# Kernel optimization log

Measured on AMD Instinct MI355X. Metric: run time of the kernel, lower is better.

Reference implementation:

```python
import jax, jax.numpy as jnp
import numpy as np
from jax import lax

B, T, N, HID = 4, 144, 256, 64
CH, NC = 9, 4  # chunk_size_short, num_chunks_short


def setup_inputs():
    key = jax.random.key(0)
    ks = jax.random.split(key, 30)
    r = lambda i, sh, s=0.05: jax.random.normal(ks[i], sh, jnp.float32) * s
    adj = (jax.random.uniform(ks[1], (N, N)) < 0.1).astype(jnp.float32)
    adj = adj.at[jnp.arange(N), jnp.arange(N)].set(1.0)  # self-loops
    return {
        "seg": jax.random.normal(ks[0], (B, T, N, N), jnp.float32),
        "adj": adj,
        "dist": jax.random.uniform(ks[2], (N, N), jnp.float32),
        "W_gat": r(3, (N, HID)),
        "a_src": r(4, (HID,)),
        "a_dst": r(5, (HID,)),
        "lstm_Wih": r(6, (4 * HID, HID)),
        "lstm_Whh": r(7, (4 * HID, HID)),
        "lstm_bih": r(8, (4 * HID,)),
        "lstm_bhh": r(9, (4 * HID,)),
        "attnL_W": r(10, (HID, HID)),
        "attnL_b": r(11, (HID,)),
        "attnL_v": r(12, (HID,)),
        "gru_Wih": r(13, (NC, 3 * HID, HID)),
        "gru_Whh": r(14, (NC, 3 * HID, HID)),
        "gru_bih": r(15, (NC, 3 * HID)),
        "gru_bhh": r(16, (NC, 3 * HID)),
        "attnS_W": r(17, (NC, HID, HID)),
        "attnS_b": r(18, (NC, HID)),
        "attnS_v": r(19, (NC, HID)),
        "lin1_W": r(20, (2 * HID, HID + HID * NC)),
        "lin1_b": r(21, (2 * HID,)),
        "lin2_W": r(22, (N * N, 2 * HID)),
        "lin2_b": r(23, (N * N,)),
        "conv_k": r(24, (1, 1, 3, 3)),
        "conv_b": r(25, (1,)),
    }


def gat_features(seg, adj, dist, W_gat, a_src, a_dst):
    # Batches the per-timestep GAT over the time axis (B,T folded together).
    Wh = jnp.einsum('btnf,fh->btnh', seg, W_gat)                     # (B,T,N,H)
    e = jax.nn.leaky_relu((Wh @ a_src)[..., :, None] + (Wh @ a_dst)[..., None, :], 0.2)
    e = e - dist                                                     # distance penalty on logits
    logits = jnp.where(adj > 0, e, -1e9)                             # mask non-edges
    attn = jax.nn.softmax(logits, axis=-1)                           # (B,T,N,N)
    Hn = jax.nn.elu(jnp.einsum('btij,btjh->btih', attn, Wh))         # (B,T,N,H)
    return Hn.mean(axis=2)                                           # (B,T,H) mean-pool over nodes


def lstm(x, Wih, Whh, bih, bhh):
    h0 = jnp.zeros((x.shape[0], Whh.shape[1]), x.dtype)
    def step(carry, xt):
        h, c = carry
        g = xt @ Wih.T + bih + h @ Whh.T + bhh
        i, f, gg, o = jnp.split(g, 4, axis=-1)  # torch gate order i,f,g,o
        c = jax.nn.sigmoid(f) * c + jax.nn.sigmoid(i) * jnp.tanh(gg)
        h = jax.nn.sigmoid(o) * jnp.tanh(c)
        return (h, c), h
    _, ys = lax.scan(step, (h0, h0), jnp.swapaxes(x, 0, 1))
    return jnp.swapaxes(ys, 0, 1)


def gru(x, Wih, Whh, bih, bhh):
    h0 = jnp.zeros((x.shape[0], Whh.shape[1]), x.dtype)
    def step(h, xt):
        gx = xt @ Wih.T + bih
        gh = h @ Whh.T + bhh
        xr, xz, xn = jnp.split(gx, 3, axis=-1)  # torch gate order r,z,n
        hr, hz, hn = jnp.split(gh, 3, axis=-1)
        rr = jax.nn.sigmoid(xr + hr)
        zz = jax.nn.sigmoid(xz + hz)
        nn_ = jnp.tanh(xn + rr * hn)
        h = (1.0 - zz) * nn_ + zz * h
        return h, h
    _, ys = lax.scan(step, h0, jnp.swapaxes(x, 0, 1))
    return jnp.swapaxes(ys, 0, 1)


def tattn(h, W, b, v):
    s = jnp.tanh(h @ W + b) @ v          # (B,T) additive attention scores
    a = jax.nn.softmax(s, axis=1)
    return jnp.einsum('bt,bth->bh', a, h)


def reference(seg, adj, dist, W_gat, a_src, a_dst, lstm_Wih, lstm_Whh, lstm_bih, lstm_bhh,
              attnL_W, attnL_b, attnL_v, gru_Wih, gru_Whh, gru_bih, gru_bhh,
              attnS_W, attnS_b, attnS_v, lin1_W, lin1_b, lin2_W, lin2_b, conv_k, conv_b):
    Bsz = seg.shape[0]
    feats = gat_features(seg, adj, dist, W_gat, a_src, a_dst)        # (B,T,H)
    ctxL = tattn(lstm(feats, lstm_Wih, lstm_Whh, lstm_bih, lstm_bhh), attnL_W, attnL_b, attnL_v)
    # Short-term GCN features are the same GAT outputs on the last W_short steps.
    short = feats[:, -CH * NC:, :].reshape(Bsz, NC, CH, HID)
    gru_out = jax.vmap(gru, in_axes=(1, 0, 0, 0, 0), out_axes=1)(short, gru_Wih, gru_Whh, gru_bih, gru_bhh)
    ctxS = jax.vmap(tattn, in_axes=(1, 0, 0, 0), out_axes=1)(gru_out, attnS_W, attnS_b, attnS_v)  # (B,NC,H)
    fused = jnp.concatenate([ctxL, ctxS.reshape(Bsz, NC * HID)], axis=1)  # (B, 5H)
    h1 = jax.nn.relu(fused @ lin1_W.T + lin1_b)
    out = (h1 @ lin2_W.T + lin2_b).reshape(Bsz, 1, N, N)
    out = lax.conv_general_dilated(out, conv_k, (1, 1), 'SAME',
                                   dimension_numbers=('NCHW', 'OIHW', 'NCHW'))
    out = out + conv_b[None, :, None, None]
    return jax.nn.softplus(out[:, 0])
```

## Files before the change

### kernel.cpp

```cpp
#include <hip/hip_runtime.h>
#include <hip/hip_bf16.h>
#include <cstddef>


typedef __attribute__((ext_vector_type(8))) short bf16x8;
typedef __attribute__((ext_vector_type(4))) float f32x4;

__device__ __forceinline__ float sigf(float x) { return 1.0f / (1.0f + __expf(-x)); }
__device__ __forceinline__ float tanh_(float x) {
    x = fminf(fmaxf(x, -15.f), 15.f);
    float e = __expf(2.f * x);
    return (e - 1.f) / (e + 1.f);
}
__device__ __forceinline__ unsigned short f2b(float f) {
    unsigned u = __float_as_uint(f);
    u += 0x7FFFu + ((u >> 16) & 1u);
    return (unsigned short)(u >> 16);
}
__device__ __forceinline__ unsigned pk2(float lo, float hi) {
    __hip_bfloat162 h = __float22bfloat162_rn(float2{lo, hi});
    return *reinterpret_cast<unsigned*>(&h);
}
__device__ __forceinline__ float b2f(short s) {
    return __uint_as_float(((unsigned)(unsigned short)s) << 16);
}

__global__ void k_prep(const float* __restrict__ adj, const float* __restrict__ dist,
                       const float* __restrict__ W_gat,
                       unsigned short* __restrict__ Mb, unsigned short* __restrict__ Wt) {
    int blk = blockIdx.x, tid = threadIdx.x;
    if (blk < 256) {
        int i = blk * 256 + tid;
        Mb[i] = f2b((adj[i] > 0.f) ? -dist[i] : -1e9f);
    } else {
        for (int it = 0; it < 64; ++it) {
            int e = it * 256 + tid;
            int k = e >> 6, c = e & 63;
            Wt[c * 256 + k] = f2b(W_gat[e]);
        }
    }
}

__global__ __launch_bounds__(256, 3) void k_gat(
    const float* __restrict__ seg, const unsigned short* __restrict__ Wt,
    const float* __restrict__ a_src, const float* __restrict__ a_dst,
    const unsigned short* __restrict__ Mb, float* __restrict__ feats,
    const float* __restrict__ lWih, const float* __restrict__ lbih,
    const float* __restrict__ lbhh, float* __restrict__ gx) {
    __shared__ __align__(16) short AB_s[256 * 64];
    __shared__ __align__(16) float svec[256];
    __shared__ __align__(16) float dvec[256];
    __shared__ __align__(16) float red[256];
    __shared__ __align__(16) float feats_l[64];

    const int tid  = threadIdx.x;
    const int lane = tid & 63;
    const int wv   = tid >> 6;
    const int wrow = wv * 64;
    const int bt   = blockIdx.x;
    const float* __restrict__ segp = seg + (size_t)bt * 65536;

    f32x4 acc[4][4];
    #pragma unroll
    for (int a = 0; a < 4; ++a)
        #pragma unroll
        for (int b = 0; b < 4; ++b) acc[a][b] = (f32x4)(0.f);

    for (int kc = 0; kc < 4; ++kc) {
        #pragma unroll
        for (int it = 0; it < 8; ++it) {
            int unit = it * 256 + tid;
            int row = unit >> 3, u = unit & 7;
            const float* g = segp + row * 256 + kc * 64 + u * 8;
            f32x4 v0 = *(const f32x4*)g;
            f32x4 v1 = *(const f32x4*)(g + 4);
            uint4 pk;
            pk.x = pk2(v0[0], v0[1]); pk.y = pk2(v0[2], v0[3]);
            pk.z = pk2(v1[0], v1[1]); pk.w = pk2(v1[2], v1[3]);
            *(uint4*)&AB_s[(row * 8 + (u ^ (row & 7))) * 8] = pk;
        }
        bf16x8 bfr[2][4];
        #pragma unroll
        for (int kt2 = 0; kt2 < 2; ++kt2) {
            int ku = kt2 * 4 + (lane >> 4);
            #pragma unroll
            for (int nt = 0; nt < 4; ++nt) {
                int col = nt * 16 + (lane & 15);
                bfr[kt2][nt] = *(const bf16x8*)(Wt + col * 256 + kc * 64 + ku * 8);
            }
        }
        __syncthreads();
        #pragma unroll
        for (int kt2 = 0; kt2 < 2; ++kt2) {
            int ku = kt2 * 4 + (lane >> 4);
            #pragma unroll
            for (int mt = 0; mt < 4; ++mt) {
                int row = wrow + mt * 16 + (lane & 15);
                bf16x8 afr = *(const bf16x8*)&AB_s[(row * 8 + (ku ^ (row & 7))) * 8];
                #pragma unroll
                for (int nt = 0; nt < 4; ++nt)
                    acc[mt][nt] = __builtin_amdgcn_mfma_f32_16x16x32_bf16(afr, bfr[kt2][nt], acc[mt][nt], 0, 0, 0);
            }
        }
        __syncthreads();
    }

    float asv[4], adv[4];
    #pragma unroll
    for (int nt = 0; nt < 4; ++nt) {
        asv[nt] = a_src[nt * 16 + (lane & 15)];
        adv[nt] = a_dst[nt * 16 + (lane & 15)];
    }
    #pragma unroll
    for (int mt = 0; mt < 4; ++mt) {
        #pragma unroll
        for (int r = 0; r < 4; ++r) {
            float ps = acc[mt][0][r] * asv[0] + acc[mt][1][r] * asv[1]
                     + acc[mt][2][r] * asv[2] + acc[mt][3][r] * asv[3];
            float pd = acc[mt][0][r] * adv[0] + acc[mt][1][r] * adv[1]
                     + acc[mt][2][r] * adv[2] + acc[mt][3][r] * adv[3];
            #pragma unroll
            for (int m = 1; m < 16; m <<= 1) {
                ps += __shfl_xor(ps, m);
                pd += __shfl_xor(pd, m);
            }
            if ((lane & 15) == 0) {
                int row = wrow + mt * 16 + (lane >> 4) * 4 + r;
                svec[row] = ps;
                dvec[row] = pd;
            }
        }
        #pragma unroll
        for (int nt = 0; nt < 4; ++nt) {
            int col  = nt * 16 + (lane & 15);
            int row0 = wrow + mt * 16 + (lane >> 4) * 4;
            uint2 pk4;
            pk4.x = pk2(acc[mt][nt][0], acc[mt][nt][1]);
            pk4.y = pk2(acc[mt][nt][2], acc[mt][nt][3]);
            int addr16 = col * 32 + ((row0 >> 3) ^ (col & 7));
            *(uint2*)&AB_s[addr16 * 8 + (row0 & 7)] = pk4;
        }
    }
    __syncthreads();

    {
        float a = svec[tid], b = dvec[tid];
        #pragma unroll
        for (int m = 1; m < 64; m <<= 1) {
            a = fmaxf(a, __shfl_xor(a, m));
            b = fmaxf(b, __shfl_xor(b, m));
        }
        if (lane == 0) { red[wv] = a; red[4 + wv] = b; }
    }
    __syncthreads();
    float mB;
    {
        float ms = fmaxf(fmaxf(red[0], red[1]), fmaxf(red[2], red[3]));
        float md = fmaxf(fmaxf(red[4], red[5]), fmaxf(red[6], red[7]));
        float x = ms + md;
        mB = fmaxf(x, 0.2f * x);
    }

    f32x4 acc2[4][4];
    #pragma unroll
    for (int a = 0; a < 4; ++a)
        #pragma unroll
        for (int b = 0; b < 4; ++b) acc2[a][b] = (f32x4)(0.f);
    float psum[4] = {0.f, 0.f, 0.f, 0.f};
    float sv4[4];
    #pragma unroll
    for (int mt = 0; mt < 4; ++mt) sv4[mt] = svec[wrow + mt * 16 + (lane & 15)];
    const int jbase = (lane >> 4) * 8;
    #pragma unroll 1
    for (int kt = 0; kt < 8; ++kt) {
        int j0 = kt * 32 + jbase;
        int ku = kt * 4 + (lane >> 4);
        bf16x8 bfr2[4];
        #pragma unroll
        for (int nt = 0; nt < 4; ++nt) {
            int col = nt * 16 + (lane & 15);
            bfr2[nt] = *(const bf16x8*)&AB_s[(col * 32 + (ku ^ (col & 7))) * 8];
        }
        f32x4 dv0 = *(const f32x4*)&dvec[j0];
        f32x4 dv1 = *(const f32x4*)&dvec[j0 + 4];
        #pragma unroll
        for (int mt = 0; mt < 4; ++mt) {
            int row = wrow + mt * 16 + (lane & 15);
            bf16x8 mrow = *(const bf16x8*)(Mb + row * 256 + j0);
            float p[8];
            #pragma unroll
            for (int e = 0; e < 4; ++e) {
                float u = sv4[mt] + dv0[e];
                u = fmaxf(u, 0.2f * u);
                p[e] = __expf(u + b2f(mrow[e]) - mB);
                float w = sv4[mt] + dv1[e];
                w = fmaxf(w, 0.2f * w);
                p[4 + e] = __expf(w + b2f(mrow[4 + e]) - mB);
            }
            psum[mt] += ((p[0] + p[1]) + (p[2] + p[3])) + ((p[4] + p[5]) + (p[6] + p[7]));
            uint4 upf;
            upf.x = pk2(p[0], p[1]); upf.y = pk2(p[2], p[3]);
            upf.z = pk2(p[4], p[5]); upf.w = pk2(p[6], p[7]);
            bf16x8 pf = *reinterpret_cast<bf16x8*>(&upf);
            #pragma unroll
            for (int nt = 0; nt < 4; ++nt)
                acc2[mt][nt] = __builtin_amdgcn_mfma_f32_16x16x32_bf16(pf, bfr2[nt], acc2[mt][nt], 0, 0, 0);
        }
    }
    #pragma unroll
    for (int mt = 0; mt < 4; ++mt) {
        psum[mt] += __shfl_xor(psum[mt], 16);
        psum[mt] += __shfl_xor(psum[mt], 32);
    }

    float part[4] = {0.f, 0.f, 0.f, 0.f};
    #pragma unroll
    for (int mt = 0; mt < 4; ++mt) {
        #pragma unroll
        for (int r = 0; r < 4; ++r) {
            float rs  = __shfl(psum[mt], ((lane >> 4) << 2) + r);
            float inv = 1.0f / rs;
            #pragma unroll
            for (int nt = 0; nt < 4; ++nt) {
                float x = acc2[mt][nt][r] * inv;
                x = (x > 0.f) ? x : expm1f(x);
                part[nt] += x;
            }
        }
    }
    #pragma unroll
    for (int nt = 0; nt < 4; ++nt) {
        part[nt] += __shfl_xor(part[nt], 16);
        part[nt] += __shfl_xor(part[nt], 32);
    }
    if ((lane >> 4) == 0) {
        #pragma unroll
        for (int nt = 0; nt < 4; ++nt) red[wv * 64 + nt * 16 + lane] = part[nt];
    }
    __syncthreads();
    if (tid < 64) {
        float f = (red[tid] + red[64 + tid] + red[128 + tid] + red[192 + tid]) * (1.0f / 256.0f);
        feats[bt * 64 + tid] = f;
        feats_l[tid] = f;
    }
    __syncthreads();

    {
        float a = lbih[tid] + lbhh[tid];
        const float* wp = lWih + tid * 64;
        #pragma unroll
        for (int k4 = 0; k4 < 16; ++k4) {
            f32x4 w = *(const f32x4*)(wp + k4 * 4);
            f32x4 x = *(const f32x4*)&feats_l[k4 * 4];
            a += w[0] * x[0] + w[1] * x[1] + w[2] * x[2] + w[3] * x[3];
        }
        gx[bt * 256 + tid] = a;
    }
}

__global__ __launch_bounds__(256) void k_rnn(
    const float* __restrict__ gx, const float* __restrict__ lWhh, float* __restrict__ lout,
    const float* __restrict__ feats, const float* __restrict__ gWih,
    const float* __restrict__ gWhh, const float* __restrict__ gbih,
    const float* __restrict__ gbhh, float* __restrict__ gout) {
    int tid = threadIdx.x;
    if (blockIdx.x < 4) {
        int b = blockIdx.x;
        int lane = tid & 63, wv = tid >> 6;
        __shared__ __align__(16) float hv[4][64];
        __shared__ __align__(16) float gl[2][256];
        float wr[64];
        #pragma unroll
        for (int q = 0; q < 16; ++q)
            *(f32x4*)&wr[q * 4] = *(const f32x4*)&lWhh[tid * 64 + q * 4];
        float c_s = 0.f;
        hv[wv][lane] = 0.f;
        for (int t = 0; t < 144; ++t) {
            float a = gx[(b * 144 + t) * 256 + tid];
            #pragma unroll
            for (int q = 0; q < 16; ++q) {
                f32x4 h4 = *(const f32x4*)&hv[wv][q * 4];
                a += wr[q * 4 + 0] * h4[0] + wr[q * 4 + 1] * h4[1]
                   + wr[q * 4 + 2] * h4[2] + wr[q * 4 + 3] * h4[3];
            }
            gl[t & 1][tid] = a;
            __syncthreads();
            float ig = gl[t & 1][lane],       fg = gl[t & 1][64 + lane],
                  gg = gl[t & 1][128 + lane], og = gl[t & 1][192 + lane];
            c_s = sigf(fg) * c_s + sigf(ig) * tanh_(gg);
            float h = sigf(og) * tanh_(c_s);
            hv[wv][lane] = h;
            if (wv == 0) lout[(b * 144 + t) * 64 + lane] = h;
        }
    } else {
        int bi_ = blockIdx.x - 4;
        int b = bi_ >> 2, c2 = bi_ & 3;
        __shared__ float hvg[64], xvg[64], gxl[192], ghl[192];
        float wi[64], wh[64], bi = 0.f, bh = 0.f, h_s = 0.f;
        if (tid < 192) {
            #pragma unroll
            for (int q = 0; q < 16; ++q) {
                *(f32x4*)&wi[q * 4] = *(const f32x4*)&gWih[(size_t)(c2 * 192 + tid) * 64 + q * 4];
                *(f32x4*)&wh[q * 4] = *(const f32x4*)&gWhh[(size_t)(c2 * 192 + tid) * 64 + q * 4];
            }
            bi = gbih[c2 * 192 + tid];
            bh = gbhh[c2 * 192 + tid];
        }
        if (tid < 64) hvg[tid] = 0.f;
        __syncthreads();
        for (int s = 0; s < 9; ++s) {
            int t = 108 + c2 * 9 + s;
            if (tid < 64) xvg[tid] = feats[(b * 144 + t) * 64 + tid];
            __syncthreads();
            if (tid < 192) {
                float ax = bi, ah = bh;
                #pragma unroll
                for (int k = 0; k < 64; ++k) { ax += wi[k] * xvg[k]; ah += wh[k] * hvg[k]; }
                gxl[tid] = ax; ghl[tid] = ah;
            }
            __syncthreads();
            if (tid < 64) {
                float xr = gxl[tid], xz = gxl[64 + tid], xn = gxl[128 + tid];
                float hr = ghl[tid], hz = ghl[64 + tid], hn = ghl[128 + tid];
                float rr = sigf(xr + hr), zz = sigf(xz + hz);
                float nn = tanh_(xn + rr * hn);
                h_s = (1.f - zz) * nn + zz * h_s;
                hvg[tid] = h_s;
                gout[((b * 4 + c2) * 9 + s) * 64 + tid] = h_s;
            }
            __syncthreads();
        }
    }
}

__global__ __launch_bounds__(256) void k_ctx(
    const float* __restrict__ lout, const float* __restrict__ aLW,
    const float* __restrict__ aLb, const float* __restrict__ aLv,
    const float* __restrict__ gout, const float* __restrict__ aSW,
    const float* __restrict__ aSb, const float* __restrict__ aSv,
    float* __restrict__ ctxL, float* __restrict__ ctxS) {
    int tid = threadIdx.x;
    if (blockIdx.x < 4) {
        int b = blockIdx.x;
        int wv = tid >> 6, lane = tid & 63;
        __shared__ __align__(16) float Hl[144 * 64];
        __shared__ float sc[144];
        __shared__ float al[144];
        for (int i = tid; i < 9216; i += 256) Hl[i] = lout[b * 9216 + i];
        float wcol[64];
        #pragma unroll
        for (int k = 0; k < 64; ++k) wcol[k] = aLW[k * 64 + lane];
        float bb = aLb[lane], vv = aLv[lane];
        __syncthreads();
        for (int g = 0; g < 36; ++g) {
            int t = g * 4 + wv;
            float acc = bb;
            #pragma unroll
            for (int q = 0; q < 16; ++q) {
                f32x4 h4 = *(const f32x4*)&Hl[t * 64 + q * 4];
                acc += wcol[q * 4 + 0] * h4[0] + wcol[q * 4 + 1] * h4[1]
                     + wcol[q * 4 + 2] * h4[2] + wcol[q * 4 + 3] * h4[3];
            }
            float p = tanh_(acc) * vv;
            #pragma unroll
            for (int m = 1; m < 64; m <<= 1) p += __shfl_xor(p, m);
            if (lane == 0) sc[t] = p;
        }
        __syncthreads();
        float mx = -3e38f;
        for (int t2 = 0; t2 < 144; ++t2) mx = fmaxf(mx, sc[t2]);
        float ss = 0.f;
        for (int t2 = 0; t2 < 144; ++t2) ss += __expf(sc[t2] - mx);
        float inv = 1.f / ss;
        if (tid < 144) al[tid] = __expf(sc[tid] - mx) * inv;
        __syncthreads();
        if (tid < 64) {
            float acc = 0.f;
            for (int t2 = 0; t2 < 144; ++t2) acc += al[t2] * Hl[t2 * 64 + tid];
            ctxL[b * 64 + tid] = acc;
        }
    } else {
        int bi_ = blockIdx.x - 4;
        int b = bi_ >> 2, c2 = bi_ & 3;
        __shared__ float xv2[64];
        if (tid < 64) {
            int lane = tid;
            const float* Wc = aSW + c2 * 4096;
            float wcol[64];
            #pragma unroll
            for (int k = 0; k < 64; ++k) wcol[k] = Wc[k * 64 + lane];
            float bb = aSb[c2 * 64 + lane], vv = aSv[c2 * 64 + lane];
            float sv[9], hl[9];
            #pragma unroll 1
            for (int s = 0; s < 9; ++s) {
                float h = gout[((size_t)((b * 4 + c2) * 9 + s)) * 64 + lane];
                hl[s] = h;
                xv2[lane] = h;
                float acc = bb;
                #pragma unroll
                for (int k = 0; k < 64; ++k) acc += wcol[k] * xv2[k];
                float p = tanh_(acc) * vv;
                #pragma unroll
                for (int m = 1; m < 64; m <<= 1) p += __shfl_xor(p, m);
                sv[s] = p;
            }
            float mx = -3e38f;
            #pragma unroll
            for (int s = 0; s < 9; ++s) mx = fmaxf(mx, sv[s]);
            float ss = 0.f;
            #pragma unroll
            for (int s = 0; s < 9; ++s) { sv[s] = __expf(sv[s] - mx); ss += sv[s]; }
            float inv = 1.f / ss;
            float acc = 0.f;
            #pragma unroll
            for (int s = 0; s < 9; ++s) acc += sv[s] * inv * hl[s];
            ctxS[(b * 4 + c2) * 64 + lane] = acc;
        }
    }
}

__global__ __launch_bounds__(512) void k_lin1(
    const float* __restrict__ ctxL, const float* __restrict__ ctxS,
    const float* __restrict__ W, const float* __restrict__ bb,
    float* __restrict__ h1) {
    int tid = threadIdx.x;
    __shared__ __align__(16) float fu[4 * 320];
    for (int c = tid; c < 1280; c += 512) {
        int b2 = c / 320, k = c % 320;
        fu[c] = (k < 64) ? ctxL[b2 * 64 + k] : ctxS[b2 * 256 + (k - 64)];
    }
    __syncthreads();
    int b = tid >> 7, r = tid & 127;
    float acc = bb[r];
    #pragma unroll 4
    for (int k4 = 0; k4 < 80; ++k4) {
        f32x4 w = *(const f32x4*)&W[r * 320 + k4 * 4];
        f32x4 x = *(const f32x4*)&fu[b * 320 + k4 * 4];
        acc += w[0] * x[0] + w[1] * x[1] + w[2] * x[2] + w[3] * x[3];
    }
    h1[b * 128 + r] = fmaxf(acc, 0.f);
}

__global__ __launch_bounds__(256) void k_lin2(
    const float* __restrict__ h1, const float* __restrict__ W,
    const float* __restrict__ bb, float* __restrict__ h2) {
    int tid = threadIdx.x, blk = blockIdx.x;
    __shared__ __align__(16) float Wc[128 * 132];
    __shared__ __align__(16) float h1l[512];
    __shared__ __align__(16) float red2[512];
    for (int c = tid; c < 512; c += 256) h1l[c] = h1[c];
    #pragma unroll
    for (int it = 0; it < 16; ++it) {
        int flat = it * 1024 + tid * 4;
        int row = flat >> 7, col = flat & 127;
        f32x4 v = *(const f32x4*)&W[(size_t)(blk * 128 + row) * 128 + col];
        *(f32x4*)&Wc[row * 132 + col] = v;
    }
    __syncthreads();
    int r2 = tid >> 1, half = tid & 1;
    float a0 = 0.f, a1 = 0.f, a2 = 0.f, a3 = 0.f;
    #pragma unroll
    for (int i = 0; i < 16; ++i) {
        f32x4 w = *(const f32x4*)&Wc[r2 * 132 + half * 64 + i * 4];
        f32x4 x0 = *(const f32x4*)&h1l[half * 64 + i * 4];
        f32x4 x1 = *(const f32x4*)&h1l[128 + half * 64 + i * 4];
        f32x4 x2 = *(const f32x4*)&h1l[256 + half * 64 + i * 4];
        f32x4 x3 = *(const f32x4*)&h1l[384 + half * 64 + i * 4];
        a0 += w[0] * x0[0] + w[1] * x0[1] + w[2] * x0[2] + w[3] * x0[3];
        a1 += w[0] * x1[0] + w[1] * x1[1] + w[2] * x1[2] + w[3] * x1[3];
        a2 += w[0] * x2[0] + w[1] * x2[1] + w[2] * x2[2] + w[3] * x2[3];
        a3 += w[0] * x3[0] + w[1] * x3[1] + w[2] * x3[2] + w[3] * x3[3];
    }
    if (half == 1) {
        f32x4 v; v[0] = a0; v[1] = a1; v[2] = a2; v[3] = a3;
        *(f32x4*)&red2[r2 * 4] = v;
    }
    __syncthreads();
    if (half == 0) {
        f32x4 v = *(const f32x4*)&red2[r2 * 4];
        int r = blk * 128 + r2;
        float bv = bb[r];
        h2[r]              = a0 + v[0] + bv;
        h2[65536 + r]      = a1 + v[1] + bv;
        h2[2 * 65536 + r]  = a2 + v[2] + bv;
        h2[3 * 65536 + r]  = a3 + v[3] + bv;
    }
}

__global__ __launch_bounds__(256) void k_conv(
    const float* __restrict__ h2, const float* __restrict__ ck,
    const float* __restrict__ cb, float* __restrict__ out) {
    int x = threadIdx.x;
    int b = blockIdx.x >> 8, y = blockIdx.x & 255;
    float kk[9];
    #pragma unroll
    for (int i = 0; i < 9; ++i) kk[i] = ck[i];
    const float* base = h2 + b * 65536;
    float acc = cb[0];
    #pragma unroll
    for (int dy = -1; dy <= 1; ++dy) {
        int yy = y + dy;
        if (yy < 0 || yy > 255) continue;
        #pragma unroll
        for (int dx = -1; dx <= 1; ++dx) {
            int xx = x + dx;
            if (xx < 0 || xx > 255) continue;
            acc += base[yy * 256 + xx] * kk[(dy + 1) * 3 + (dx + 1)];
        }
    }
    float r = (acc > 20.f) ? acc : log1pf(__expf(acc));
    out[b * 65536 + y * 256 + x] = r;
}

extern "C" void kernel_launch(void* const* d_in, const int* in_sizes, int n_in,
                              void* d_out, int out_size, void* d_ws, size_t ws_size,
                              hipStream_t stream) {
    const float* seg   = (const float*)d_in[0];
    const float* adj   = (const float*)d_in[1];
    const float* dist  = (const float*)d_in[2];
    const float* W_gat = (const float*)d_in[3];
    const float* a_src = (const float*)d_in[4];
    const float* a_dst = (const float*)d_in[5];
    const float* lWih  = (const float*)d_in[6];
    const float* lWhh  = (const float*)d_in[7];
    const float* lbih  = (const float*)d_in[8];
    const float* lbhh  = (const float*)d_in[9];
    const float* aLW   = (const float*)d_in[10];
    const float* aLb   = (const float*)d_in[11];
    const float* aLv   = (const float*)d_in[12];
    const float* gWih  = (const float*)d_in[13];
    const float* gWhh  = (const float*)d_in[14];
    const float* gbih  = (const float*)d_in[15];
    const float* gbhh  = (const float*)d_in[16];
    const float* aSW   = (const float*)d_in[17];
    const float* aSb   = (const float*)d_in[18];
    const float* aSv   = (const float*)d_in[19];
    const float* l1W   = (const float*)d_in[20];
    const float* l1b   = (const float*)d_in[21];
    const float* l2W   = (const float*)d_in[22];
    const float* l2b   = (const float*)d_in[23];
    const float* ck    = (const float*)d_in[24];
    const float* cb    = (const float*)d_in[25];
    float* out = (float*)d_out;

    float* ws    = (float*)d_ws;
    unsigned short* Mb = (unsigned short*)ws;
    float* feats = ws + 32768;
    float* gx    = feats + 36864;
    float* lout  = gx + 147456;
    float* ctxL  = lout + 36864;
    float* gout  = ctxL + 256;
    float* ctxS  = gout + 9216;
    float* h1    = ctxS + 1024;
    float* h2    = h1 + 512;
    unsigned short* Wt = (unsigned short*)(h2 + 262144);

    k_prep<<<257, 256, 0, stream>>>(adj, dist, W_gat, Mb, Wt);
    k_gat<<<576, 256, 0, stream>>>(seg, Wt, a_src, a_dst, Mb, feats, lWih, lbih, lbhh, gx);
    k_rnn<<<20, 256, 0, stream>>>(gx, lWhh, lout, feats, gWih, gWhh, gbih, gbhh, gout);
    k_ctx<<<20, 256, 0, stream>>>(lout, aLW, aLb, aLv, gout, aSW, aSb, aSv, ctxL, ctxS);
    k_lin1<<<1, 512, 0, stream>>>(ctxL, ctxS, l1W, l1b, h1);
    k_lin2<<<512, 256, 0, stream>>>(h1, l2W, l2b, h2);
    k_conv<<<1024, 256, 0, stream>>>(h2, ck, cb, out);
}
```

Before: 236.2 us.

## Split GAT kernel into row-block projection and attention kernels, tweak RNN and lin2

Splits the fused per-timestep GAT kernel into k_gatA (projection of 64 rows per block, writing Wh transposed plus source/destination scores and partial maxima to global memory) and k_gatB (attention aggregation of 64 rows per block). A new k_feats kernel reduces the four partial pools and applies the LSTM input projection. The aim is to raise the block count from 576 to 2304 and cut per-block LDS and register use so more blocks fit per CU. The cost is global round-trips for Wh and the score vectors plus two extra launches. It also prefetches gx and splits accumulators in the LSTM/GRU loops, and makes lin2 read weights directly from global with shuffle reductions instead of staging through LDS.

Result: slower. 272.1 us (+15.2%).

```diff
diff --git a/kernel.cpp b/kernel.cpp
--- a/kernel.cpp
+++ b/kernel.cpp
@@ -41,34 +41,29 @@
     }
 }
 
-__global__ __launch_bounds__(256, 3) void k_gat(
+__global__ __launch_bounds__(256, 6) void k_gatA(
     const float* __restrict__ seg, const unsigned short* __restrict__ Wt,
     const float* __restrict__ a_src, const float* __restrict__ a_dst,
-    const unsigned short* __restrict__ Mb, float* __restrict__ feats,
-    const float* __restrict__ lWih, const float* __restrict__ lbih,
-    const float* __restrict__ lbhh, float* __restrict__ gx) {
-    __shared__ __align__(16) short AB_s[256 * 64];
-    __shared__ __align__(16) float svec[256];
-    __shared__ __align__(16) float dvec[256];
-    __shared__ __align__(16) float red[256];
-    __shared__ __align__(16) float feats_l[64];
+    unsigned short* __restrict__ WhT, float* __restrict__ svec, float* __restrict__ dvec,
+    float* __restrict__ smaxp, float* __restrict__ dmaxp) {
+    __shared__ __align__(16) short A_s[64 * 64];
+    __shared__ float red[8];
 
     const int tid  = threadIdx.x;
     const int lane = tid & 63;
     const int wv   = tid >> 6;
-    const int wrow = wv * 64;
-    const int bt   = blockIdx.x;
-    const float* __restrict__ segp = seg + (size_t)bt * 65536;
-
-    f32x4 acc[4][4];
-    #pragma unroll
-    for (int a = 0; a < 4; ++a)
-        #pragma unroll
-        for (int b = 0; b < 4; ++b) acc[a][b] = (f32x4)(0.f);
+    const int blk  = blockIdx.x;
+    const int bt   = blk >> 2;
+    const int sub  = blk & 3;
+    const float* __restrict__ segp = seg + (size_t)bt * 65536 + sub * 64 * 256;
+
+    f32x4 acc[4];
+    #pragma unroll
+    for (int n = 0; n < 4; ++n) acc[n] = (f32x4)(0.f);
 
     for (int kc = 0; kc < 4; ++kc) {
         #pragma unroll
-        for (int it = 0; it < 8; ++it) {
+        for (int it = 0; it < 2; ++it) {
             int unit = it * 256 + tid;
             int row = unit >> 3, u = unit & 7;
             const float* g = segp + row * 256 + kc * 64 + u * 8;
@@ -77,7 +72,7 @@
             uint4 pk;
             pk.x = pk2(v0[0], v0[1]); pk.y = pk2(v0[2], v0[3]);
             pk.z = pk2(v1[0], v1[1]); pk.w = pk2(v1[2], v1[3]);
-            *(uint4*)&AB_s[(row * 8 + (u ^ (row & 7))) * 8] = pk;
+            *(uint4*)&A_s[(row * 8 + (u ^ (row & 7))) * 8] = pk;
         }
         bf16x8 bfr[2][4];
         #pragma unroll
@@ -90,17 +85,14 @@
             }
         }
         __syncthreads();
+        int arow = wv * 16 + (lane & 15);
         #pragma unroll
         for (int kt2 = 0; kt2 < 2; ++kt2) {
             int ku = kt2 * 4 + (lane >> 4);
-            #pragma unroll
-            for (int mt = 0; mt < 4; ++mt) {
-                int row = wrow + mt * 16 + (lane & 15);
-                bf16x8 afr = *(const bf16x8*)&AB_s[(row * 8 + (ku ^ (row & 7))) * 8];
-                #pragma unroll
-                for (int nt = 0; nt < 4; ++nt)
-                    acc[mt][nt] = __builtin_amdgcn_mfma_f32_16x16x32_bf16(afr, bfr[kt2][nt], acc[mt][nt], 0, 0, 0);
-            }
+            bf16x8 afr = *(const bf16x8*)&A_s[(arow * 8 + (ku ^ (arow & 7))) * 8];
+            #pragma unroll
+            for (int nt = 0; nt < 4; ++nt)
+                acc[nt] = __builtin_amdgcn_mfma_f32_16x16x32_bf16(afr, bfr[kt2][nt], acc[nt], 0, 0, 0);
         }
         __syncthreads();
     }
@@ -111,121 +103,123 @@
         asv[nt] = a_src[nt * 16 + (lane & 15)];
         adv[nt] = a_dst[nt * 16 + (lane & 15)];
     }
-    #pragma unroll
-    for (int mt = 0; mt < 4; ++mt) {
-        #pragma unroll
-        for (int r = 0; r < 4; ++r) {
-            float ps = acc[mt][0][r] * asv[0] + acc[mt][1][r] * asv[1]
-                     + acc[mt][2][r] * asv[2] + acc[mt][3][r] * asv[3];
-            float pd = acc[mt][0][r] * adv[0] + acc[mt][1][r] * adv[1]
-                     + acc[mt][2][r] * adv[2] + acc[mt][3][r] * adv[3];
-            #pragma unroll
-            for (int m = 1; m < 16; m <<= 1) {
-                ps += __shfl_xor(ps, m);
-                pd += __shfl_xor(pd, m);
-            }
-            if ((lane & 15) == 0) {
-                int row = wrow + mt * 16 + (lane >> 4) * 4 + r;
-                svec[row] = ps;
-                dvec[row] = pd;
-            }
-        }
+    float mxs = -3e38f, mxd = -3e38f;
+    int rowbase = sub * 64 + wv * 16;
+    #pragma unroll
+    for (int r = 0; r < 4; ++r) {
+        float ps = acc[0][r] * asv[0] + acc[1][r] * asv[1] + acc[2][r] * asv[2] + acc[3][r] * asv[3];
+        float pd = acc[0][r] * adv[0] + acc[1][r] * adv[1] + acc[2][r] * adv[2] + acc[3][r] * adv[3];
+        #pragma unroll
+        for (int m = 1; m < 16; m <<= 1) { ps += __shfl_xor(ps, m); pd += __shfl_xor(pd, m); }
+        if ((lane & 15) == 0) {
+            int row = rowbase + (lane >> 4) * 4 + r;
+            svec[bt * 256 + row] = ps;
+            dvec[bt * 256 + row] = pd;
+        }
+        mxs = fmaxf(mxs, ps); mxd = fmaxf(mxd, pd);
+    }
+    {
+        unsigned short* Wp = WhT + (size_t)bt * 16384;
+        int row0 = rowbase + (lane >> 4) * 4;
         #pragma unroll
         for (int nt = 0; nt < 4; ++nt) {
-            int col  = nt * 16 + (lane & 15);
-            int row0 = wrow + mt * 16 + (lane >> 4) * 4;
+            int col = nt * 16 + (lane & 15);
             uint2 pk4;
-            pk4.x = pk2(acc[mt][nt][0], acc[mt][nt][1]);
-            pk4.y = pk2(acc[mt][nt][2], acc[mt][nt][3]);
-            int addr16 = col * 32 + ((row0 >> 3) ^ (col & 7));
-            *(uint2*)&AB_s[addr16 * 8 + (row0 & 7)] = pk4;
-        }
-    }
+            pk4.x = pk2(acc[nt][0], acc[nt][1]);
+            pk4.y = pk2(acc[nt][2], acc[nt][3]);
+            *(uint2*)(Wp + col * 256 + row0) = pk4;
+        }
+    }
+    mxs = fmaxf(mxs, __shfl_xor(mxs, 16)); mxs = fmaxf(mxs, __shfl_xor(mxs, 32));
+    mxd = fmaxf(mxd, __shfl_xor(mxd, 16)); mxd = fmaxf(mxd, __shfl_xor(mxd, 32));
+    if (lane == 0) { red[wv] = mxs; red[4 + wv] = mxd; }
     __syncthreads();
-
-    {
-        float a = svec[tid], b = dvec[tid];
-        #pragma unroll
-        for (int m = 1; m < 64; m <<= 1) {
-            a = fmaxf(a, __shfl_xor(a, m));
-            b = fmaxf(b, __shfl_xor(b, m));
-        }
-        if (lane == 0) { red[wv] = a; red[4 + wv] = b; }
-    }
-    __syncthreads();
+    if (tid == 0) {
+        smaxp[blk] = fmaxf(fmaxf(red[0], red[1]), fmaxf(red[2], red[3]));
+        dmaxp[blk] = fmaxf(fmaxf(red[4], red[5]), fmaxf(red[6], red[7]));
+    }
+}
+
+__global__ __launch_bounds__(256, 4) void k_gatB(
+    const unsigned short* __restrict__ WhT, const float* __restrict__ svec,
+    const float* __restrict__ dvec, const float* __restrict__ smaxp,
+    const float* __restrict__ dmaxp, const unsigned short* __restrict__ Mb,
+    float* __restrict__ fpart) {
+    __shared__ __align__(16) float dv_l[256];
+    __shared__ float red[256];
+
+    const int tid  = threadIdx.x;
+    const int lane = tid & 63;
+    const int wv   = tid >> 6;
+    const int blk  = blockIdx.x;
+    const int bt   = blk >> 2;
+    const int sub  = blk & 3;
+    const unsigned short* __restrict__ Wp = WhT + (size_t)bt * 16384;
+
+    dv_l[tid] = dvec[bt * 256 + tid];
     float mB;
     {
-        float ms = fmaxf(fmaxf(red[0], red[1]), fmaxf(red[2], red[3]));
-        float md = fmaxf(fmaxf(red[4], red[5]), fmaxf(red[6], red[7]));
+        float ms = fmaxf(fmaxf(smaxp[bt * 4], smaxp[bt * 4 + 1]),
+                         fmaxf(smaxp[bt * 4 + 2], smaxp[bt * 4 + 3]));
+        float md = fmaxf(fmaxf(dmaxp[bt * 4], dmaxp[bt * 4 + 1]),
+                         fmaxf(dmaxp[bt * 4 + 2], dmaxp[bt * 4 + 3]));
         float x = ms + md;
         mB = fmaxf(x, 0.2f * x);
     }
-
-    f32x4 acc2[4][4];
-    #pragma unroll
-    for (int a = 0; a < 4; ++a)
-        #pragma unroll
-        for (int b = 0; b < 4; ++b) acc2[a][b] = (f32x4)(0.f);
-    float psum[4] = {0.f, 0.f, 0.f, 0.f};
-    float sv4[4];
-    #pragma unroll
-    for (int mt = 0; mt < 4; ++mt) sv4[mt] = svec[wrow + mt * 16 + (lane & 15)];
+    const int prow = sub * 64 + wv * 16 + (lane & 15);
+    const float sv = svec[bt * 256 + prow];
+    __syncthreads();
+
+    f32x4 acc2[4];
+    #pragma unroll
+    for (int n = 0; n < 4; ++n) acc2[n] = (f32x4)(0.f);
+    float psum = 0.f;
     const int jbase = (lane >> 4) * 8;
+
     #pragma unroll 1
     for (int kt = 0; kt < 8; ++kt) {
         int j0 = kt * 32 + jbase;
-        int ku = kt * 4 + (lane >> 4);
-        bf16x8 bfr2[4];
+        bf16x8 bfr[4];
         #pragma unroll
         for (int nt = 0; nt < 4; ++nt) {
             int col = nt * 16 + (lane & 15);
-            bfr2[nt] = *(const bf16x8*)&AB_s[(col * 32 + (ku ^ (col & 7))) * 8];
-        }
-        f32x4 dv0 = *(const f32x4*)&dvec[j0];
-        f32x4 dv1 = *(const f32x4*)&dvec[j0 + 4];
-        #pragma unroll
-        for (int mt = 0; mt < 4; ++mt) {
-            int row = wrow + mt * 16 + (lane & 15);
-            bf16x8 mrow = *(const bf16x8*)(Mb + row * 256 + j0);
-            float p[8];
-            #pragma unroll
-            for (int e = 0; e < 4; ++e) {
-                float u = sv4[mt] + dv0[e];
-                u = fmaxf(u, 0.2f * u);
-                p[e] = __expf(u + b2f(mrow[e]) - mB);
-                float w = sv4[mt] + dv1[e];
-                w = fmaxf(w, 0.2f * w);
-                p[4 + e] = __expf(w + b2f(mrow[4 + e]) - mB);
-            }
-            psum[mt] += ((p[0] + p[1]) + (p[2] + p[3])) + ((p[4] + p[5]) + (p[6] + p[7]));
-            uint4 upf;
-            upf.x = pk2(p[0], p[1]); upf.y = pk2(p[2], p[3]);
-            upf.z = pk2(p[4], p[5]); upf.w = pk2(p[6], p[7]);
-            bf16x8 pf = *reinterpret_cast<bf16x8*>(&upf);
-            #pragma unroll
-            for (int nt = 0; nt < 4; ++nt)
-                acc2[mt][nt] = __builtin_amdgcn_mfma_f32_16x16x32_bf16(pf, bfr2[nt], acc2[mt][nt], 0, 0, 0);
-        }
-    }
-    #pragma unroll
-    for (int mt = 0; mt < 4; ++mt) {
-        psum[mt] += __shfl_xor(psum[mt], 16);
-        psum[mt] += __shfl_xor(psum[mt], 32);
-    }
+            bfr[nt] = *(const bf16x8*)(Wp + col * 256 + j0);
+        }
+        bf16x8 mrow = *(const bf16x8*)(Mb + prow * 256 + j0);
+        f32x4 d0 = *(const f32x4*)&dv_l[j0];
+        f32x4 d1 = *(const f32x4*)&dv_l[j0 + 4];
+        float p[8];
+        #pragma unroll
+        for (int e = 0; e < 4; ++e) {
+            float u = sv + d0[e];
+            u = fmaxf(u, 0.2f * u);
+            p[e] = __expf(u + b2f(mrow[e]) - mB);
+            float w = sv + d1[e];
+            w = fmaxf(w, 0.2f * w);
+            p[4 + e] = __expf(w + b2f(mrow[4 + e]) - mB);
+        }
+        psum += ((p[0] + p[1]) + (p[2] + p[3])) + ((p[4] + p[5]) + (p[6] + p[7]));
+        uint4 upf;
+        upf.x = pk2(p[0], p[1]); upf.y = pk2(p[2], p[3]);
+        upf.z = pk2(p[4], p[5]); upf.w = pk2(p[6], p[7]);
+        bf16x8 pf = *reinterpret_cast<bf16x8*>(&upf);
+        #pragma unroll
+        for (int nt = 0; nt < 4; ++nt)
+            acc2[nt] = __builtin_amdgcn_mfma_f32_16x16x32_bf16(pf, bfr[nt], acc2[nt], 0, 0, 0);
+    }
+    psum += __shfl_xor(psum, 16);
+    psum += __shfl_xor(psum, 32);
 
     float part[4] = {0.f, 0.f, 0.f, 0.f};
     #pragma unroll
-    for (int mt = 0; mt < 4; ++mt) {
-        #pragma unroll
-        for (int r = 0; r < 4; ++r) {
-            float rs  = __shfl(psum[mt], ((lane >> 4) << 2) + r);
-            float inv = 1.0f / rs;
-            #pragma unroll
-            for (int nt = 0; nt < 4; ++nt) {
-                float x = acc2[mt][nt][r] * inv;
-                x = (x > 0.f) ? x : expm1f(x);
-                part[nt] += x;
-            }
+    for (int r = 0; r < 4; ++r) {
+        float rs  = __shfl(psum, ((lane >> 4) << 2) + r);
+        float inv = 1.0f / rs;
+        #pragma unroll
+        for (int nt = 0; nt < 4; ++nt) {
+            float x = acc2[nt][r] * inv;
+            x = (x > 0.f) ? x : expm1f(x);
+            part[nt] += x;
         }
     }
     #pragma unroll
@@ -238,24 +232,32 @@
         for (int nt = 0; nt < 4; ++nt) red[wv * 64 + nt * 16 + lane] = part[nt];
     }
     __syncthreads();
+    if (tid < 64)
+        fpart[blk * 64 + tid] = red[tid] + red[64 + tid] + red[128 + tid] + red[192 + tid];
+}
+
+__global__ __launch_bounds__(256) void k_feats(
+    const float* __restrict__ fpart, const float* __restrict__ lWih,
+    const float* __restrict__ lbih, const float* __restrict__ lbhh,
+    float* __restrict__ feats, float* __restrict__ gx) {
+    __shared__ __align__(16) float fl[64];
+    int bt = blockIdx.x, tid = threadIdx.x;
     if (tid < 64) {
-        float f = (red[tid] + red[64 + tid] + red[128 + tid] + red[192 + tid]) * (1.0f / 256.0f);
+        float f = (fpart[(bt * 4 + 0) * 64 + tid] + fpart[(bt * 4 + 1) * 64 + tid]
+                 + fpart[(bt * 4 + 2) * 64 + tid] + fpart[(bt * 4 + 3) * 64 + tid]) * (1.0f / 256.0f);
         feats[bt * 64 + tid] = f;
-        feats_l[tid] = f;
+        fl[tid] = f;
     }
     __syncthreads();
-
-    {
-        float a = lbih[tid] + lbhh[tid];
-        const float* wp = lWih + tid * 64;
-        #pragma unroll
-        for (int k4 = 0; k4 < 16; ++k4) {
-            f32x4 w = *(const f32x4*)(wp + k4 * 4);
-            f32x4 x = *(const f32x4*)&feats_l[k4 * 4];
-            a += w[0] * x[0] + w[1] * x[1] + w[2] * x[2] + w[3] * x[3];
-        }
-        gx[bt * 256 + tid] = a;
-    }
+    float a = lbih[tid] + lbhh[tid];
+    const float* wp = lWih + tid * 64;
+    #pragma unroll
+    for (int k4 = 0; k4 < 16; ++k4) {
+        f32x4 w = *(const f32x4*)(wp + k4 * 4);
+        f32x4 x = *(const f32x4*)&fl[k4 * 4];
+        a += w[0] * x[0] + w[1] * x[1] + w[2] * x[2] + w[3] * x[3];
+    }
+    gx[bt * 256 + tid] = a;
 }
 
 __global__ __launch_bounds__(256) void k_rnn(
@@ -275,14 +277,22 @@
             *(f32x4*)&wr[q * 4] = *(const f32x4*)&lWhh[tid * 64 + q * 4];
         float c_s = 0.f;
         hv[wv][lane] = 0.f;
+        float gx_cur = gx[(size_t)b * 144 * 256 + tid];
         for (int t = 0; t < 144; ++t) {
-            float a = gx[(b * 144 + t) * 256 + tid];
-            #pragma unroll
-            for (int q = 0; q < 16; ++q) {
-                f32x4 h4 = *(const f32x4*)&hv[wv][q * 4];
-                a += wr[q * 4 + 0] * h4[0] + wr[q * 4 + 1] * h4[1]
-                   + wr[q * 4 + 2] * h4[2] + wr[q * 4 + 3] * h4[3];
-            }
+            float gx_next = (t < 143) ? gx[((size_t)b * 144 + t + 1) * 256 + tid] : 0.f;
+            float s0 = 0.f, s1 = 0.f, s2 = 0.f, s3 = 0.f;
+            #pragma unroll
+            for (int q = 0; q < 4; ++q) {
+                f32x4 h0 = *(const f32x4*)&hv[wv][q * 16];
+                f32x4 h1 = *(const f32x4*)&hv[wv][q * 16 + 4];
+                f32x4 h2 = *(const f32x4*)&hv[wv][q * 16 + 8];
+                f32x4 h3 = *(const f32x4*)&hv[wv][q * 16 + 12];
+                s0 += wr[q*16+ 0]*h0[0] + wr[q*16+ 1]*h0[1] + wr[q*16+ 2]*h0[2] + wr[q*16+ 3]*h0[3];
+                s1 += wr[q*16+ 4]*h1[0] + wr[q*16+ 5]*h1[1] + wr[q*16+ 6]*h1[2] + wr[q*16+ 7]*h1[3];
+                s2 += wr[q*16+ 8]*h2[0] + wr[q*16+ 9]*h2[1] + wr[q*16+10]*h2[2] + wr[q*16+11]*h2[3];
+                s3 += wr[q*16+12]*h3[0] + wr[q*16+13]*h3[1] + wr[q*16+14]*h3[2] + wr[q*16+15]*h3[3];
+            }
+            float a = gx_cur + ((s0 + s1) + (s2 + s3));
             gl[t & 1][tid] = a;
             __syncthreads();
             float ig = gl[t & 1][lane],       fg = gl[t & 1][64 + lane],
@@ -291,6 +301,7 @@
             float h = sigf(og) * tanh_(c_s);
             hv[wv][lane] = h;
             if (wv == 0) lout[(b * 144 + t) * 64 + lane] = h;
+            gx_cur = gx_next;
         }
     } else {
         int bi_ = blockIdx.x - 4;
@@ -314,9 +325,13 @@
             __syncthreads();
             if (tid < 192) {
                 float ax = bi, ah = bh;
+                float a0 = 0.f, a1 = 0.f, b0 = 0.f, b1 = 0.f;
                 #pragma unroll
-                for (int k = 0; k < 64; ++k) { ax += wi[k] * xvg[k]; ah += wh[k] * hvg[k]; }
-                gxl[tid] = ax; ghl[tid] = ah;
+                for (int k = 0; k < 64; k += 2) {
+                    a0 += wi[k] * xvg[k];     a1 += wi[k + 1] * xvg[k + 1];
+                    b0 += wh[k] * hvg[k];     b1 += wh[k + 1] * hvg[k + 1];
+                }
+                gxl[tid] = ax + a0 + a1; ghl[tid] = ah + b0 + b1;
             }
             __syncthreads();
             if (tid < 64) {
@@ -444,46 +459,36 @@
 __global__ __launch_bounds__(256) void k_lin2(
     const float* __restrict__ h1, const float* __restrict__ W,
     const float* __restrict__ bb, float* __restrict__ h2) {
+    __shared__ __align__(16) float h1l[512];
     int tid = threadIdx.x, blk = blockIdx.x;
-    __shared__ __align__(16) float Wc[128 * 132];
-    __shared__ __align__(16) float h1l[512];
-    __shared__ __align__(16) float red2[512];
     for (int c = tid; c < 512; c += 256) h1l[c] = h1[c];
-    #pragma unroll
-    for (int it = 0; it < 16; ++it) {
-        int flat = it * 1024 + tid * 4;
-        int row = flat >> 7, col = flat & 127;
-        f32x4 v = *(const f32x4*)&W[(size_t)(blk * 128 + row) * 128 + col];
-        *(f32x4*)&Wc[row * 132 + col] = v;
-    }
     __syncthreads();
-    int r2 = tid >> 1, half = tid & 1;
+    int r = blk * 64 + (tid >> 2);
+    int q = tid & 3;
+    const float* wp = W + (size_t)r * 128 + q * 32;
     float a0 = 0.f, a1 = 0.f, a2 = 0.f, a3 = 0.f;
     #pragma unroll
-    for (int i = 0; i < 16; ++i) {
-        f32x4 w = *(const f32x4*)&Wc[r2 * 132 + half * 64 + i * 4];
-        f32x4 x0 = *(const f32x4*)&h1l[half * 64 + i * 4];
-        f32x4 x1 = *(const f32x4*)&h1l[128 + half * 64 + i * 4];
-        f32x4 x2 = *(const f32x4*)&h1l[256 + half * 64 + i * 4];
-        f32x4 x3 = *(const f32x4*)&h1l[384 + half * 64 + i * 4];
+    for (int i = 0; i < 8; ++i) {
+        f32x4 w  = *(const f32x4*)(wp + i * 4);
+        f32x4 x0 = *(const f32x4*)&h1l[q * 32 + i * 4];
+        f32x4 x1 = *(const f32x4*)&h1l[128 + q * 32 + i * 4];
+        f32x4 x2 = *(const f32x4*)&h1l[256 + q * 32 + i * 4];
+        f32x4 x3 = *(const f32x4*)&h1l[384 + q * 32 + i * 4];
         a0 += w[0] * x0[0] + w[1] * x0[1] + w[2] * x0[2] + w[3] * x0[3];
         a1 += w[0] * x1[0] + w[1] * x1[1] + w[2] * x1[2] + w[3] * x1[3];
         a2 += w[0] * x2[0] + w[1] * x2[1] + w[2] * x2[2] + w[3] * x2[3];
         a3 += w[0] * x3[0] + w[1] * x3[1] + w[2] * x3[2] + w[3] * x3[3];
     }
-    if (half == 1) {
-        f32x4 v; v[0] = a0; v[1] = a1; v[2] = a2; v[3] = a3;
-        *(f32x4*)&red2[r2 * 4] = v;
-    }
-    __syncthreads();
-    if (half == 0) {
-        f32x4 v = *(const f32x4*)&red2[r2 * 4];
-        int r = blk * 128 + r2;
+    a0 += __shfl_xor(a0, 1); a0 += __shfl_xor(a0, 2);
+    a1 += __shfl_xor(a1, 1); a1 += __shfl_xor(a1, 2);
+    a2 += __shfl_xor(a2, 1); a2 += __shfl_xor(a2, 2);
+    a3 += __shfl_xor(a3, 1); a3 += __shfl_xor(a3, 2);
+    if (q == 0) {
         float bv = bb[r];
-        h2[r]              = a0 + v[0] + bv;
-        h2[65536 + r]      = a1 + v[1] + bv;
-        h2[2 * 65536 + r]  = a2 + v[2] + bv;
-        h2[3 * 65536 + r]  = a3 + v[3] + bv;
+        h2[r]             = a0 + bv;
+        h2[65536 + r]     = a1 + bv;
+        h2[2 * 65536 + r] = a2 + bv;
+        h2[3 * 65536 + r] = a3 + bv;
     }
 }
 
@@ -543,23 +548,31 @@
     const float* cb    = (const float*)d_in[25];
     float* out = (float*)d_out;
 
-    float* ws    = (float*)d_ws;
-    unsigned short* Mb = (unsigned short*)ws;
-    float* feats = ws + 32768;
+    float* ws = (float*)d_ws;
+    unsigned short* Mb  = (unsigned short*)ws;
+    unsigned short* Wt  = (unsigned short*)(ws + 32768);
+    float* svec  = ws + 40960;
+    float* dvec  = svec + 147456;
+    float* smaxp = dvec + 147456;
+    float* dmaxp = smaxp + 2304;
+    unsigned short* WhT = (unsigned short*)(dmaxp + 2304);
+    float* fpart = dmaxp + 2304 + 4718592;
+    float* feats = fpart + 147456;
     float* gx    = feats + 36864;
     float* lout  = gx + 147456;
-    float* ctxL  = lout + 36864;
-    float* gout  = ctxL + 256;
-    float* ctxS  = gout + 9216;
+    float* gout  = lout + 36864;
+    float* ctxL  = gout + 9216;
+    float* ctxS  = ctxL + 256;
     float* h1    = ctxS + 1024;
     float* h2    = h1 + 512;
-    unsigned short* Wt = (unsigned short*)(h2 + 262144);
 
     k_prep<<<257, 256, 0, stream>>>(adj, dist, W_gat, Mb, Wt);
-    k_gat<<<576, 256, 0, stream>>>(seg, Wt, a_src, a_dst, Mb, feats, lWih, lbih, lbhh, gx);
+    k_gatA<<<2304, 256, 0, stream>>>(seg, Wt, a_src, a_dst, WhT, svec, dvec, smaxp, dmaxp);
+    k_gatB<<<2304, 256, 0, stream>>>(WhT, svec, dvec, smaxp, dmaxp, Mb, fpart);
+    k_feats<<<576, 256, 0, stream>>>(fpart, lWih, lbih, lbhh, feats, gx);
     k_rnn<<<20, 256, 0, stream>>>(gx, lWhh, lout, feats, gWih, gWhh, gbih, gbhh, gout);
     k_ctx<<<20, 256, 0, stream>>>(lout, aLW, aLb, aLv, gout, aSW, aSb, aSv, ctxL, ctxS);
     k_lin1<<<1, 512, 0, stream>>>(ctxL, ctxS, l1W, l1b, h1);
-    k_lin2<<<512, 256, 0, stream>>>(h1, l2W, l2b, h2);
+    k_lin2<<<1024, 256, 0, stream>>>(h1, l2W, l2b, h2);
     k_conv<<<1024, 256, 0, stream>>>(h2, ck, cb, out);
 }
```
